# Optimization experiments

Hardware: AMD Instinct MI355X
Metric: run time of the kernel (lower is better)

## Reference

```python
import jax, jax.numpy as jnp
import numpy as np

D_MODEL = 2048
N_HEADS = 16
HEAD_DIM = D_MODEL // N_HEADS
SEQ = 2048
THETA = 10000.0


def rope_tables(head_dim, context_length, theta=THETA):
    inv_freq = 1.0 / theta ** (jnp.arange(0, head_dim, 2, dtype=jnp.float32) / head_dim)
    angles = jnp.arange(context_length, dtype=jnp.float32)[:, None] * inv_freq[None, :]
    angles = jnp.concatenate([angles, angles], axis=1)  # [S, head_dim]
    return jnp.cos(angles), jnp.sin(angles)


def apply_rope(x, cos, sin):
    # x: [B, H, S, Dh]; cos/sin: [S, Dh]
    half = x.shape[-1] // 2
    x1, x2 = x[..., :half], x[..., half:]
    rotated = jnp.concatenate([-x2, x1], axis=-1)
    return x * cos[None, None] + rotated * sin[None, None]


def setup_inputs() -> dict:
    key = jax.random.key(0)
    ks = jax.random.split(key, 5)
    s = 1.0 / np.sqrt(D_MODEL)
    x = jax.random.normal(ks[0], (2, SEQ, D_MODEL), dtype=jnp.float32)
    Wq = jax.random.normal(ks[1], (D_MODEL, D_MODEL), dtype=jnp.float32) * s
    Wk = jax.random.normal(ks[2], (D_MODEL, D_MODEL), dtype=jnp.float32) * s
    Wv = jax.random.normal(ks[3], (D_MODEL, D_MODEL), dtype=jnp.float32) * s
    Wo = jax.random.normal(ks[4], (D_MODEL, D_MODEL), dtype=jnp.float32) * s
    return {"x": x, "Wq": Wq, "Wk": Wk, "Wv": Wv, "Wo": Wo}


def reference(x, Wq, Wk, Wv, Wo):
    B, S, D = x.shape
    cos, sin = rope_tables(HEAD_DIM, SEQ)
    cos, sin = cos[:S], sin[:S]

    def split_heads(t):  # [B,S,D] -> [B,H,S,Dh]
        return t.reshape(B, S, N_HEADS, HEAD_DIM).transpose(0, 2, 1, 3)

    q = apply_rope(split_heads(x @ Wq.T), cos, sin)
    k = apply_rope(split_heads(x @ Wk.T), cos, sin)
    v = split_heads(x @ Wv.T)

    scores = jnp.einsum('bhqd,bhkd->bhqk', q, k) / np.sqrt(HEAD_DIM).astype(np.float32)
    causal = jnp.tril(jnp.ones((S, S), dtype=bool))
    scores = jnp.where(causal[None, None], scores, -jnp.inf)
    weights = jax.nn.softmax(scores, axis=-1)
    ctx = jnp.einsum('bhqk,bhkd->bhqd', weights, v)
    ctx = ctx.transpose(0, 2, 1, 3).reshape(B, S, D)
    return ctx @ Wo.T
```

## Files before the change

kernel.cpp:

```cpp
#include <hip/hip_runtime.h>
#include <hip/hip_bf16.h>
#include <cstdint>
#include <cstddef>

typedef __bf16 bf16;
typedef __bf16 bf16x4 __attribute__((ext_vector_type(4)));
typedef __bf16 bf16x8 __attribute__((ext_vector_type(8)));
typedef float f32x4 __attribute__((ext_vector_type(4)));

#define D_MODEL 2048
#define SEQ     2048
#define NH      16
#define HD      128
#define BATCH   2
#define QKV_LD  6144

#define SBAR()  __builtin_amdgcn_sched_barrier(0)
#define HWBAR() do { SBAR(); __builtin_amdgcn_s_barrier(); SBAR(); } while (0)

__device__ __forceinline__ void gld16(void* lds, const void* g) {
    __builtin_amdgcn_global_load_lds(
        (const __attribute__((address_space(1))) unsigned int*)g,
        (__attribute__((address_space(3))) unsigned int*)lds,
        16, 0, 0);
}

__global__ __launch_bounds__(256) void cvt_f32_bf16(const float* __restrict__ in,
                                                    bf16* __restrict__ out, int n) {
    int i = (blockIdx.x * 256 + threadIdx.x) * 4;
    if (i < n) {
        float4 v = *(const float4*)(in + i);
        out[i + 0] = (bf16)v.x;
        out[i + 1] = (bf16)v.y;
        out[i + 2] = (bf16)v.z;
        out[i + 3] = (bf16)v.w;
    }
}

__global__ __launch_bounds__(256) void rope_tables_k(float* __restrict__ cosd,
                                                     float* __restrict__ sind) {
    int id = blockIdx.x * 256 + threadIdx.x;
    int s = id >> 6, d = id & 63;
    float freq = powf(10000.f, -(float)d * (1.f / 64.f));
    float a = (float)s * freq;
    float sn, c;
    sincosf(a, &sn, &c);
    cosd[id] = c;
    sind[id] = sn;
}

__global__ __launch_bounds__(256) void rope_apply(bf16* __restrict__ T,
                                                  const float* __restrict__ cosd,
                                                  const float* __restrict__ sind,
                                                  float scale, int ld) {
    int id = blockIdx.x * 256 + threadIdx.x;
    int row = id >> 10;
    int p = id & 1023;
    int h = p >> 6, d = p & 63;
    int s = row & (SEQ - 1);
    size_t base = (size_t)row * ld + h * HD + d;
    float x1 = (float)T[base];
    float x2 = (float)T[base + 64];
    float c = cosd[(s << 6) + d];
    float sn = sind[(s << 6) + d];
    T[base]      = (bf16)((x1 * c - x2 * sn) * scale);
    T[base + 64] = (bf16)((x2 * c + x1 * sn) * scale);
}

__global__ __launch_bounds__(256) void transpose_v(const bf16* __restrict__ V,
                                                   bf16* __restrict__ Vt, int ld) {
    __shared__ bf16 t[32][33];
    int s0 = blockIdx.x * 32;
    int d0 = blockIdx.y * 32;
    int bh = blockIdx.z;
    int b = bh >> 4, h = bh & 15;
    int tx = threadIdx.x & 31, ty = threadIdx.x >> 5;
#pragma unroll
    for (int i = 0; i < 32; i += 8)
        t[ty + i][tx] = V[((size_t)(b * SEQ + s0 + ty + i)) * ld + h * HD + d0 + tx];
    __syncthreads();
#pragma unroll
    for (int i = 0; i < 32; i += 8)
        Vt[((size_t)bh * HD + d0 + ty + i) * SEQ + s0 + tx] = t[tx][ty + i];
}

template <int OUTF32>
__global__ __launch_bounds__(512, 2)
void gemm8p(const bf16* __restrict__ A, const bf16* __restrict__ B,
            void* __restrict__ Cout, int M, int N, int K) {
    __shared__ __align__(16) bf16 ldsAB[2][2][2][128 * 64];

    const int nN = N >> 8;
    const int nwg = gridDim.x;
    const int cpx = nwg >> 3;
    const int lin = (blockIdx.x & 7) * cpx + (blockIdx.x >> 3);
    const int m0 = (lin / nN) * 256, n0 = (lin % nN) * 256;

    const int tid = threadIdx.x;
    const int w = tid >> 6, l = tid & 63;
    const int wm = w >> 2, wn = w & 3;
    const int lg = l >> 4, lc = l & 15;
    const int swz = (lc & 7) << 4;
    const int NT = K >> 6;
    const int HMAX = NT * 4;

    f32x4 acc[2][2][4][2] = {};

    auto stage = [&](int H) {
        const int tau = H >> 2, h = H & 3;
        bf16* dst = &ldsAB[tau & 1][h >> 1][h & 1][0];
#pragma unroll
        for (int j = 0; j < 2; ++j) {
            int r = w * 8 + j * 64 + (l >> 3);
            int scb = ((l & 7) * 16) ^ ((r & 7) << 4);
            const bf16* g = (h < 2)
                ? A + (size_t)(m0 + (h & 1) * 128 + r) * K + tau * 64 + (scb >> 1)
                : B + (size_t)(n0 + (h & 1) * 128 + r) * K + tau * 64 + (scb >> 1);
            gld16(dst + (w * 8 + j * 64) * 64, g);
        }
    };

    stage(0); stage(1); stage(2); stage(3); stage(4);
    SBAR();
    asm volatile("s_waitcnt vmcnt(2)" ::: "memory");
    HWBAR();

    for (int t = 0; t < NT; ++t) {
        const int c = t & 1;
        const char* Ab = (const char*)&ldsAB[c][0][wm][0];
        const char* Bb = (const char*)&ldsAB[c][1][wn >> 1][0];
        const int brow0 = (wn & 1) * 64;
        bf16x8 Af[4][2], Bf[2][2][2];

#pragma unroll
        for (int mt = 0; mt < 4; ++mt)
#pragma unroll
            for (int ks = 0; ks < 2; ++ks)
                Af[mt][ks] = *(const bf16x8*)(Ab + (mt * 16 + lc) * 128 + ((ks * 64 + lg * 16) ^ swz));
#pragma unroll
        for (int nt = 0; nt < 2; ++nt)
#pragma unroll
            for (int ks = 0; ks < 2; ++ks)
                Bf[0][nt][ks] = *(const bf16x8*)(Bb + (brow0 + nt * 16 + lc) * 128 + ((ks * 64 + lg * 16) ^ swz));
        { int H = 4 * t + 5; if (H < HMAX) stage(H); }
        HWBAR();
        __builtin_amdgcn_s_setprio(1);
#pragma unroll
        for (int mt = 0; mt < 4; ++mt)
#pragma unroll
            for (int nt = 0; nt < 2; ++nt)
#pragma unroll
                for (int ks = 0; ks < 2; ++ks)
                    acc[0][0][mt][nt] = __builtin_amdgcn_mfma_f32_16x16x32_bf16(Af[mt][ks], Bf[0][nt][ks], acc[0][0][mt][nt], 0, 0, 0);
        __builtin_amdgcn_s_setprio(0);
        HWBAR();

#pragma unroll
        for (int nt = 0; nt < 2; ++nt)
#pragma unroll
            for (int ks = 0; ks < 2; ++ks)
                Bf[1][nt][ks] = *(const bf16x8*)(Bb + (brow0 + 32 + nt * 16 + lc) * 128 + ((ks * 64 + lg * 16) ^ swz));
        { int H = 4 * t + 6; if (H < HMAX) stage(H); }
        HWBAR();
        __builtin_amdgcn_s_setprio(1);
#pragma unroll
        for (int mt = 0; mt < 4; ++mt)
#pragma unroll
            for (int nt = 0; nt < 2; ++nt)
#pragma unroll
                for (int ks = 0; ks < 2; ++ks)
                    acc[0][1][mt][nt] = __builtin_amdgcn_mfma_f32_16x16x32_bf16(Af[mt][ks], Bf[1][nt][ks], acc[0][1][mt][nt], 0, 0, 0);
        __builtin_amdgcn_s_setprio(0);
        HWBAR();

#pragma unroll
        for (int mt = 0; mt < 4; ++mt)
#pragma unroll
            for (int ks = 0; ks < 2; ++ks)
                Af[mt][ks] = *(const bf16x8*)(Ab + (64 + mt * 16 + lc) * 128 + ((ks * 64 + lg * 16) ^ swz));
        { int H = 4 * t + 7; if (H < HMAX) stage(H); }
        HWBAR();
        __builtin_amdgcn_s_setprio(1);
#pragma unroll
        for (int mt = 0; mt < 4; ++mt)
#pragma unroll
            for (int nt = 0; nt < 2; ++nt)
#pragma unroll
                for (int ks = 0; ks < 2; ++ks)
                    acc[1][0][mt][nt] = __builtin_amdgcn_mfma_f32_16x16x32_bf16(Af[mt][ks], Bf[0][nt][ks], acc[1][0][mt][nt], 0, 0, 0);
        __builtin_amdgcn_s_setprio(0);
        HWBAR();

        { int H = 4 * t + 8; if (H < HMAX) stage(H); }
        HWBAR();
        __builtin_amdgcn_s_setprio(1);
#pragma unroll
        for (int mt = 0; mt < 4; ++mt)
#pragma unroll
            for (int nt = 0; nt < 2; ++nt)
#pragma unroll
                for (int ks = 0; ks < 2; ++ks)
                    acc[1][1][mt][nt] = __builtin_amdgcn_mfma_f32_16x16x32_bf16(Af[mt][ks], Bf[1][nt][ks], acc[1][1][mt][nt], 0, 0, 0);
        __builtin_amdgcn_s_setprio(0);
        SBAR();
        asm volatile("s_waitcnt vmcnt(2)" ::: "memory");
        HWBAR();
    }

#pragma unroll
    for (int mq = 0; mq < 2; ++mq)
#pragma unroll
        for (int nq = 0; nq < 2; ++nq)
#pragma unroll
            for (int mt = 0; mt < 4; ++mt)
#pragma unroll
                for (int nt = 0; nt < 2; ++nt)
#pragma unroll
                    for (int rr = 0; rr < 4; ++rr) {
                        size_t row = (size_t)m0 + wm * 128 + mq * 64 + mt * 16 + lg * 4 + rr;
                        size_t col = (size_t)n0 + wn * 64 + nq * 32 + nt * 16 + lc;
                        float v = acc[mq][nq][mt][nt][rr];
                        if (OUTF32) ((float*)Cout)[row * N + col] = v;
                        else        ((bf16*)Cout)[row * N + col] = (bf16)v;
                    }
}

__global__ __launch_bounds__(256)
void flash_attn(const bf16* __restrict__ QKV, const bf16* __restrict__ Vt,
                bf16* __restrict__ O) {
    __shared__ __align__(16) bf16 Ks[2][64 * 128];
    __shared__ __align__(16) bf16 Vs[2][128 * 64];
    __shared__ __align__(16) bf16 p_lds[4][16 * 64];

    const int bid = blockIdx.x;
    const int lin = (bid & 7) * 64 + (bid >> 3);
    const int bh = lin >> 4;
    const int jj = lin & 15;
    const int b = bh >> 4, h = bh & 15;

    const int tid = threadIdx.x;
    const int w = tid >> 6, l = tid & 63;
    const int lg = l >> 4, lc = l & 15;
    const int kswz = (lc & 7) << 4;
    char* pb = (char*)&p_lds[w][0];

    auto stageK = [&](int p, int kb) {
#pragma unroll
        for (int c = 0; c < 4; ++c) {
            int r = c * 16 + w * 4 + (l >> 4);
            int scb = ((l & 15) * 16) ^ ((r & 7) << 4);
            const bf16* g = QKV + ((size_t)(b * SEQ + kb * 64 + r)) * QKV_LD + D_MODEL + h * HD + (scb >> 1);
            gld16(&Ks[p][(c * 16 + w * 4) * 128], g);
        }
    };
    auto stageV = [&](int p, int kb) {
#pragma unroll
        for (int c = 0; c < 4; ++c) {
            int r = c * 32 + w * 8 + (l >> 3);
            int scb = ((l & 7) * 16) ^ ((r & 7) << 4);
            const bf16* g = Vt + ((size_t)bh * HD + r) * SEQ + kb * 64 + (scb >> 1);
            gld16(&Vs[p][(c * 32 + w * 8) * 64], g);
        }
    };

    int cur = 0;
#pragma unroll 1
    for (int ti = 0; ti < 2; ++ti) {
        const int qt = ti ? jj : (31 - jj);
        const int q0 = qt * 64 + w * 16;

        const bf16* qp = QKV + ((size_t)(b * SEQ + q0 + lc)) * QKV_LD + h * HD + lg * 8;
        bf16x8 qf[4];
#pragma unroll
        for (int kc = 0; kc < 4; ++kc) qf[kc] = *(const bf16x8*)(qp + kc * 32);

        f32x4 ctx[8] = {};
        float m_s = -INFINITY, l_s = 0.f;

        stageK(cur, 0);
        stageV(cur, 0);

        for (int kb = 0; kb <= qt; ++kb) {
            __syncthreads();
            if (kb < qt) { stageK(cur ^ 1, kb + 1); stageV(cur ^ 1, kb + 1); }

            const char* kbp = (const char*)&Ks[cur][0];
            f32x4 st[4] = {};
#pragma unroll
            for (int nf = 0; nf < 4; ++nf) {
                int krow = nf * 16 + lc;
#pragma unroll
                for (int kc = 0; kc < 4; ++kc) {
                    bf16x8 kf = *(const bf16x8*)(kbp + krow * 256 + ((kc * 64 + lg * 16) ^ kswz));
                    st[nf] = __builtin_amdgcn_mfma_f32_16x16x32_bf16(kf, qf[kc], st[nf], 0, 0, 0);
                }
            }

            if (kb == qt) {
                int q = q0 + lc;
#pragma unroll
                for (int nf = 0; nf < 4; ++nf) {
                    int key = kb * 64 + nf * 16 + lg * 4;
#pragma unroll
                    for (int r = 0; r < 4; ++r)
                        if (key + r > q) st[nf][r] = -INFINITY;
                }
            }

            float mx = -INFINITY;
#pragma unroll
            for (int nf = 0; nf < 4; ++nf)
#pragma unroll
                for (int r = 0; r < 4; ++r) mx = fmaxf(mx, st[nf][r]);
            mx = fmaxf(mx, __shfl_xor(mx, 16));
            mx = fmaxf(mx, __shfl_xor(mx, 32));
            float mi = fmaxf(m_s, mx);
            float scv = __expf(m_s - mi);
            m_s = mi;

            float rs = 0.f;
#pragma unroll
            for (int nf = 0; nf < 4; ++nf) {
                float p0 = __expf(st[nf][0] - mi);
                float p1 = __expf(st[nf][1] - mi);
                float p2 = __expf(st[nf][2] - mi);
                float p3 = __expf(st[nf][3] - mi);
                rs += (p0 + p1) + (p2 + p3);
                bf16x4 pv = { (bf16)p0, (bf16)p1, (bf16)p2, (bf16)p3 };
                *(bf16x4*)(pb + lc * 128 + ((nf * 32 + lg * 8) ^ kswz)) = pv;
            }
            rs += __shfl_xor(rs, 16);
            rs += __shfl_xor(rs, 32);
            l_s = l_s * scv + rs;

            float scvr[4];
#pragma unroll
            for (int r = 0; r < 4; ++r) scvr[r] = __shfl(scv, lg * 4 + r);
#pragma unroll
            for (int nd = 0; nd < 8; ++nd)
#pragma unroll
                for (int r = 0; r < 4; ++r) ctx[nd][r] *= scvr[r];

            asm volatile("s_waitcnt lgkmcnt(0)" ::: "memory");
            SBAR();
            bf16x8 pa0 = *(const bf16x8*)(pb + lc * 128 + ((lg * 16) ^ kswz));
            bf16x8 pa1 = *(const bf16x8*)(pb + lc * 128 + ((64 + lg * 16) ^ kswz));

            const char* vb = (const char*)&Vs[cur][0];
#pragma unroll
            for (int nd = 0; nd < 8; ++nd) {
                int vrow = nd * 16 + lc;
#pragma unroll
                for (int k2 = 0; k2 < 2; ++k2) {
                    bf16x8 vf = *(const bf16x8*)(vb + vrow * 128 + ((k2 * 64 + lg * 16) ^ kswz));
                    ctx[nd] = __builtin_amdgcn_mfma_f32_16x16x32_bf16(k2 ? pa1 : pa0, vf, ctx[nd], 0, 0, 0);
                }
            }
            cur ^= 1;
        }

        float lr[4];
#pragma unroll
        for (int r = 0; r < 4; ++r) lr[r] = 1.f / __shfl(l_s, lg * 4 + r);
#pragma unroll
        for (int nd = 0; nd < 8; ++nd)
#pragma unroll
            for (int r = 0; r < 4; ++r)
                O[((size_t)(b * SEQ + q0 + lg * 4 + r)) * D_MODEL + h * HD + nd * 16 + lc] =
                    (bf16)(ctx[nd][r] * lr[r]);
    }
}

extern "C" void kernel_launch(void* const* d_in, const int* in_sizes, int n_in,
                              void* d_out, int out_size, void* d_ws, size_t ws_size,
                              hipStream_t stream) {
    const float* x  = (const float*)d_in[0];
    const float* Wq = (const float*)d_in[1];
    const float* Wk = (const float*)d_in[2];
    const float* Wv = (const float*)d_in[3];
    const float* Wo = (const float*)d_in[4];

    char* ws = (char*)d_ws;
    bf16* xb   = (bf16*)(ws + 0);
    bf16* wqkv = (bf16*)(ws + 16777216);
    bf16* wob  = (bf16*)(ws + 41943040);
    bf16* QKV  = (bf16*)(ws + 50331648);
    bf16* Vtb  = (bf16*)(ws + 100663296);
    float* cosd = (float*)(ws + 117440512);
    float* sind = (float*)(ws + 117964800);

    const int NX = BATCH * SEQ * D_MODEL;
    const int NW = D_MODEL * D_MODEL;

    cvt_f32_bf16<<<NX / 1024, 256, 0, stream>>>(x,  xb,  NX);
    cvt_f32_bf16<<<NW / 1024, 256, 0, stream>>>(Wq, wqkv,            NW);
    cvt_f32_bf16<<<NW / 1024, 256, 0, stream>>>(Wk, wqkv + NW,       NW);
    cvt_f32_bf16<<<NW / 1024, 256, 0, stream>>>(Wv, wqkv + 2 * NW,   NW);
    cvt_f32_bf16<<<NW / 1024, 256, 0, stream>>>(Wo, wob,             NW);

    rope_tables_k<<<(SEQ * 64) / 256, 256, 0, stream>>>(cosd, sind);

    gemm8p<0><<<dim3((QKV_LD / 256) * ((BATCH * SEQ) / 256)), 512, 0, stream>>>(
        xb, wqkv, QKV, BATCH * SEQ, QKV_LD, D_MODEL);

    const float qscale = 0.08838834764831845f;
    rope_apply<<<(BATCH * SEQ * 1024) / 256, 256, 0, stream>>>(QKV,           cosd, sind, qscale, QKV_LD);
    rope_apply<<<(BATCH * SEQ * 1024) / 256, 256, 0, stream>>>(QKV + D_MODEL, cosd, sind, 1.0f,   QKV_LD);

    transpose_v<<<dim3(SEQ / 32, HD / 32, BATCH * NH), 256, 0, stream>>>(QKV + 2 * D_MODEL, Vtb, QKV_LD);

    flash_attn<<<dim3(512), 256, 0, stream>>>(QKV, Vtb, xb );

    gemm8p<1><<<dim3((D_MODEL / 256) * ((BATCH * SEQ) / 256)), 512, 0, stream>>>(
        xb, wob, d_out, BATCH * SEQ, D_MODEL, D_MODEL);
}
```

Baseline: 296.0 us.

## Merge conversion kernels, remap GEMM tiles per XCD, restructure GEMM prefetch

Five f32-to-bf16 conversion launches become one kernel that indexes x and the four weight matrices from a single flat range; the workspace layout is contiguous, so the outputs land in the same places. The GEMM now assigns each XCD a compact rectangular block of output tiles, chosen to minimise rows plus columns, to improve L2 reuse of A and B. The staging schedule changes from one quarter-tile per phase to staging the B halves of the next k-step and the A halves two k-steps ahead. This removes a barrier and uses different vmcnt waits, which deepens the prefetch but adds pipeline-depth and synchronisation risk.

```diff
diff --git a/kernel.cpp b/kernel.cpp
--- a/kernel.cpp
+++ b/kernel.cpp
@@ -25,16 +25,25 @@
         16, 0, 0);
 }
 
-__global__ __launch_bounds__(256) void cvt_f32_bf16(const float* __restrict__ in,
-                                                    bf16* __restrict__ out, int n) {
+__global__ __launch_bounds__(256) void cvt_all(const float* __restrict__ x,
+                                               const float* __restrict__ Wq,
+                                               const float* __restrict__ Wk,
+                                               const float* __restrict__ Wv,
+                                               const float* __restrict__ Wo,
+                                               bf16* __restrict__ out) {
     int i = (blockIdx.x * 256 + threadIdx.x) * 4;
-    if (i < n) {
-        float4 v = *(const float4*)(in + i);
-        out[i + 0] = (bf16)v.x;
-        out[i + 1] = (bf16)v.y;
-        out[i + 2] = (bf16)v.z;
-        out[i + 3] = (bf16)v.w;
+    const float* src;
+    int off;
+    if (i < 8388608) { src = x; off = i; }
+    else {
+        int j = i - 8388608;
+        int seg = j >> 22;
+        src = (seg == 0) ? Wq : (seg == 1) ? Wk : (seg == 2) ? Wv : Wo;
+        off = j & 4194303;
     }
+    float4 v = *(const float4*)(src + off);
+    bf16* o = out + i;
+    o[0] = (bf16)v.x; o[1] = (bf16)v.y; o[2] = (bf16)v.z; o[3] = (bf16)v.w;
 }
 
 __global__ __launch_bounds__(256) void rope_tables_k(float* __restrict__ cosd,
@@ -90,11 +99,27 @@
             void* __restrict__ Cout, int M, int N, int K) {
     __shared__ __align__(16) bf16 ldsAB[2][2][2][128 * 64];
 
-    const int nN = N >> 8;
-    const int nwg = gridDim.x;
-    const int cpx = nwg >> 3;
-    const int lin = (blockIdx.x & 7) * cpx + (blockIdx.x >> 3);
-    const int m0 = (lin / nN) * 256, n0 = (lin % nN) * 256;
+    const int nM = M >> 8, nN = N >> 8;
+    const int cpx = (nM * nN) >> 3;
+
+    int bchm = 0, bchn = 0, best = 0x7fffffff;
+    for (int d = 1; d <= cpx; ++d) {
+        if (cpx % d) continue;
+        int cm = cpx / d;
+        if (nM % cm || nN % d) continue;
+        if (cm + d < best) { best = cm + d; bchm = cm; bchn = d; }
+    }
+    int mt0, nt0;
+    if (bchm) {
+        const int ncn = nN / bchn;
+        const int xcd = blockIdx.x & 7, loc = blockIdx.x >> 3;
+        mt0 = (xcd / ncn) * bchm + loc / bchn;
+        nt0 = (xcd % ncn) * bchn + loc % bchn;
+    } else {
+        const int lin = (blockIdx.x & 7) * cpx + (blockIdx.x >> 3);
+        mt0 = lin / nN; nt0 = lin % nN;
+    }
+    const int m0 = mt0 * 256, n0 = nt0 * 256;
 
     const int tid = threadIdx.x;
     const int w = tid >> 6, l = tid & 63;
@@ -102,27 +127,25 @@
     const int lg = l >> 4, lc = l & 15;
     const int swz = (lc & 7) << 4;
     const int NT = K >> 6;
-    const int HMAX = NT * 4;
 
     f32x4 acc[2][2][4][2] = {};
 
-    auto stage = [&](int H) {
-        const int tau = H >> 2, h = H & 3;
-        bf16* dst = &ldsAB[tau & 1][h >> 1][h & 1][0];
+    auto stageU = [&](int tau, int u) {
+        bf16* dst = &ldsAB[tau & 1][u >> 1][u & 1][0];
+        const bf16* src = (u < 2) ? A + (size_t)(m0 + (u & 1) * 128) * K
+                                  : B + (size_t)(n0 + (u & 1) * 128) * K;
 #pragma unroll
         for (int j = 0; j < 2; ++j) {
             int r = w * 8 + j * 64 + (l >> 3);
             int scb = ((l & 7) * 16) ^ ((r & 7) << 4);
-            const bf16* g = (h < 2)
-                ? A + (size_t)(m0 + (h & 1) * 128 + r) * K + tau * 64 + (scb >> 1)
-                : B + (size_t)(n0 + (h & 1) * 128 + r) * K + tau * 64 + (scb >> 1);
-            gld16(dst + (w * 8 + j * 64) * 64, g);
+            gld16(dst + (w * 8 + j * 64) * 64, src + (size_t)r * K + tau * 64 + (scb >> 1));
         }
     };
 
-    stage(0); stage(1); stage(2); stage(3); stage(4);
+    stageU(0, 0); stageU(0, 1); stageU(0, 2); stageU(0, 3);
+    stageU(1, 0); stageU(1, 1);
     SBAR();
-    asm volatile("s_waitcnt vmcnt(2)" ::: "memory");
+    asm volatile("s_waitcnt vmcnt(4)" ::: "memory");
     HWBAR();
 
     for (int t = 0; t < NT; ++t) {
@@ -142,7 +165,7 @@
 #pragma unroll
             for (int ks = 0; ks < 2; ++ks)
                 Bf[0][nt][ks] = *(const bf16x8*)(Bb + (brow0 + nt * 16 + lc) * 128 + ((ks * 64 + lg * 16) ^ swz));
-        { int H = 4 * t + 5; if (H < HMAX) stage(H); }
+        if (t + 1 < NT) stageU(t + 1, 2);
         HWBAR();
         __builtin_amdgcn_s_setprio(1);
 #pragma unroll
@@ -160,7 +183,7 @@
 #pragma unroll
             for (int ks = 0; ks < 2; ++ks)
                 Bf[1][nt][ks] = *(const bf16x8*)(Bb + (brow0 + 32 + nt * 16 + lc) * 128 + ((ks * 64 + lg * 16) ^ swz));
-        { int H = 4 * t + 6; if (H < HMAX) stage(H); }
+        if (t + 1 < NT) stageU(t + 1, 3);
         HWBAR();
         __builtin_amdgcn_s_setprio(1);
 #pragma unroll
@@ -178,7 +201,6 @@
 #pragma unroll
             for (int ks = 0; ks < 2; ++ks)
                 Af[mt][ks] = *(const bf16x8*)(Ab + (64 + mt * 16 + lc) * 128 + ((ks * 64 + lg * 16) ^ swz));
-        { int H = 4 * t + 7; if (H < HMAX) stage(H); }
         HWBAR();
         __builtin_amdgcn_s_setprio(1);
 #pragma unroll
@@ -191,8 +213,7 @@
         __builtin_amdgcn_s_setprio(0);
         HWBAR();
 
-        { int H = 4 * t + 8; if (H < HMAX) stage(H); }
-        HWBAR();
+        if (t + 2 < NT) { stageU(t + 2, 0); stageU(t + 2, 1); }
         __builtin_amdgcn_s_setprio(1);
 #pragma unroll
         for (int mt = 0; mt < 4; ++mt)
@@ -203,7 +224,8 @@
                     acc[1][1][mt][nt] = __builtin_amdgcn_mfma_f32_16x16x32_bf16(Af[mt][ks], Bf[1][nt][ks], acc[1][1][mt][nt], 0, 0, 0);
         __builtin_amdgcn_s_setprio(0);
         SBAR();
-        asm volatile("s_waitcnt vmcnt(2)" ::: "memory");
+        if (t + 2 < NT) asm volatile("s_waitcnt vmcnt(4)" ::: "memory");
+        else            asm volatile("s_waitcnt vmcnt(0)" ::: "memory");
         HWBAR();
     }
 
@@ -389,14 +411,7 @@
     float* cosd = (float*)(ws + 117440512);
     float* sind = (float*)(ws + 117964800);
 
-    const int NX = BATCH * SEQ * D_MODEL;
-    const int NW = D_MODEL * D_MODEL;
-
-    cvt_f32_bf16<<<NX / 1024, 256, 0, stream>>>(x,  xb,  NX);
-    cvt_f32_bf16<<<NW / 1024, 256, 0, stream>>>(Wq, wqkv,            NW);
-    cvt_f32_bf16<<<NW / 1024, 256, 0, stream>>>(Wk, wqkv + NW,       NW);
-    cvt_f32_bf16<<<NW / 1024, 256, 0, stream>>>(Wv, wqkv + 2 * NW,   NW);
-    cvt_f32_bf16<<<NW / 1024, 256, 0, stream>>>(Wo, wob,             NW);
+    cvt_all<<<25165824 / 1024, 256, 0, stream>>>(x, Wq, Wk, Wv, Wo, xb);
 
     rope_tables_k<<<(SEQ * 64) / 256, 256, 0, stream>>>(cosd, sind);
 
```

Result: slower. 311.0 us (+5.1%).

## Merge conversion launches, fix GEMM tail wait, use 128-tile GEMM for output projection

Applied to the files above, without the earlier changes.

Replaces the five f32-to-bf16 conversion launches with one kernel that picks the source tensor by index, relying on the workspace buffers being contiguous. Changes the final loop iteration of the pipelined GEMM to wait for all outstanding loads. Adds a simpler double-buffered 128x128 GEMM and uses it for the output projection, so that smaller GEMM gets more blocks to fill the GPU. The new GEMM has a shallower pipeline and more uncoalesced output stores, which may offset the occupancy gain.

```diff
diff --git a/kernel.cpp b/kernel.cpp
--- a/kernel.cpp
+++ b/kernel.cpp
@@ -25,16 +25,25 @@
         16, 0, 0);
 }
 
-__global__ __launch_bounds__(256) void cvt_f32_bf16(const float* __restrict__ in,
-                                                    bf16* __restrict__ out, int n) {
+__global__ __launch_bounds__(256) void cvt_all(const float* __restrict__ x,
+                                               const float* __restrict__ Wq,
+                                               const float* __restrict__ Wk,
+                                               const float* __restrict__ Wv,
+                                               const float* __restrict__ Wo,
+                                               bf16* __restrict__ out) {
     int i = (blockIdx.x * 256 + threadIdx.x) * 4;
-    if (i < n) {
-        float4 v = *(const float4*)(in + i);
-        out[i + 0] = (bf16)v.x;
-        out[i + 1] = (bf16)v.y;
-        out[i + 2] = (bf16)v.z;
-        out[i + 3] = (bf16)v.w;
+    const float* src;
+    int off;
+    if (i < 8388608) { src = x; off = i; }
+    else {
+        int j = i - 8388608;
+        int seg = j >> 22;
+        src = (seg == 0) ? Wq : (seg == 1) ? Wk : (seg == 2) ? Wv : Wo;
+        off = j & 4194303;
     }
+    float4 v = *(const float4*)(src + off);
+    bf16* o = out + i;
+    o[0] = (bf16)v.x; o[1] = (bf16)v.y; o[2] = (bf16)v.z; o[3] = (bf16)v.w;
 }
 
 __global__ __launch_bounds__(256) void rope_tables_k(float* __restrict__ cosd,
@@ -203,7 +212,8 @@
                     acc[1][1][mt][nt] = __builtin_amdgcn_mfma_f32_16x16x32_bf16(Af[mt][ks], Bf[1][nt][ks], acc[1][1][mt][nt], 0, 0, 0);
         __builtin_amdgcn_s_setprio(0);
         SBAR();
-        asm volatile("s_waitcnt vmcnt(2)" ::: "memory");
+        if (t + 2 < NT) asm volatile("s_waitcnt vmcnt(2)" ::: "memory");
+        else            asm volatile("s_waitcnt vmcnt(0)" ::: "memory");
         HWBAR();
     }
 
@@ -223,6 +233,68 @@
                         if (OUTF32) ((float*)Cout)[row * N + col] = v;
                         else        ((bf16*)Cout)[row * N + col] = (bf16)v;
                     }
+}
+
+template <int OUTF32>
+__global__ __launch_bounds__(256)
+void gemm_nt(const bf16* __restrict__ A, const bf16* __restrict__ B,
+             void* __restrict__ Cout, int M, int N, int K) {
+    __shared__ bf16 As[2][128 * 32];
+    __shared__ bf16 Bs[2][128 * 32];
+    const int m0 = blockIdx.y * 128, n0 = blockIdx.x * 128;
+    const int tid = threadIdx.x;
+    const int w = tid >> 6, l = tid & 63;
+    const int wr = w >> 1, wc = w & 1;
+    const int lg = l >> 4, lc = l & 15;
+
+    f32x4 acc[4][4] = {};
+    const int NT = K >> 5;
+
+    auto stage = [&](int p, int t) {
+#pragma unroll
+        for (int c = 0; c < 2; ++c) {
+            int reg = w * 2 + c;
+            const bf16* ga = A + (size_t)(m0 + reg * 16 + (l >> 2)) * K + t * 32 + (l & 3) * 8;
+            const bf16* gb = B + (size_t)(n0 + reg * 16 + (l >> 2)) * K + t * 32 + (l & 3) * 8;
+            gld16(&As[p][reg * 512], ga);
+            gld16(&Bs[p][reg * 512], gb);
+        }
+    };
+
+    stage(0, 0);
+    int cur = 0;
+    for (int t = 0; t < NT; ++t) {
+        __syncthreads();
+        if (t + 1 < NT) stage(cur ^ 1, t + 1);
+        bf16x8 af[4], bfr[4];
+#pragma unroll
+        for (int m = 0; m < 4; ++m)
+            af[m] = *(const bf16x8*)&As[cur][(wr * 64 + m * 16 + lc) * 32 + lg * 8];
+#pragma unroll
+        for (int n = 0; n < 4; ++n)
+            bfr[n] = *(const bf16x8*)&Bs[cur][(wc * 64 + n * 16 + lc) * 32 + lg * 8];
+#pragma unroll
+        for (int m = 0; m < 4; ++m)
+#pragma unroll
+            for (int n = 0; n < 4; ++n)
+                acc[m][n] = __builtin_amdgcn_mfma_f32_16x16x32_bf16(af[m], bfr[n], acc[m][n], 0, 0, 0);
+        cur ^= 1;
+    }
+
+#pragma unroll
+    for (int m = 0; m < 4; ++m)
+#pragma unroll
+        for (int n = 0; n < 4; ++n)
+#pragma unroll
+            for (int r = 0; r < 4; ++r) {
+                size_t row = (size_t)m0 + wr * 64 + m * 16 + lg * 4 + r;
+                size_t col = (size_t)n0 + wc * 64 + n * 16 + lc;
+                float v = acc[m][n][r];
+                if (OUTF32)
+                    ((float*)Cout)[row * N + col] = v;
+                else
+                    ((bf16*)Cout)[row * N + col] = (bf16)v;
+            }
 }
 
 __global__ __launch_bounds__(256)
@@ -389,18 +461,11 @@
     float* cosd = (float*)(ws + 117440512);
     float* sind = (float*)(ws + 117964800);
 
-    const int NX = BATCH * SEQ * D_MODEL;
-    const int NW = D_MODEL * D_MODEL;
-
-    cvt_f32_bf16<<<NX / 1024, 256, 0, stream>>>(x,  xb,  NX);
-    cvt_f32_bf16<<<NW / 1024, 256, 0, stream>>>(Wq, wqkv,            NW);
-    cvt_f32_bf16<<<NW / 1024, 256, 0, stream>>>(Wk, wqkv + NW,       NW);
-    cvt_f32_bf16<<<NW / 1024, 256, 0, stream>>>(Wv, wqkv + 2 * NW,   NW);
-    cvt_f32_bf16<<<NW / 1024, 256, 0, stream>>>(Wo, wob,             NW);
+    cvt_all<<<25165824 / 1024, 256, 0, stream>>>(x, Wq, Wk, Wv, Wo, xb);
 
     rope_tables_k<<<(SEQ * 64) / 256, 256, 0, stream>>>(cosd, sind);
 
-    gemm8p<0><<<dim3((QKV_LD / 256) * ((BATCH * SEQ) / 256)), 512, 0, stream>>>(
+    gemm8p<0><<<dim3(384), 512, 0, stream>>>(
         xb, wqkv, QKV, BATCH * SEQ, QKV_LD, D_MODEL);
 
     const float qscale = 0.08838834764831845f;
@@ -411,6 +476,6 @@
 
     flash_attn<<<dim3(512), 256, 0, stream>>>(QKV, Vtb, xb );
 
-    gemm8p<1><<<dim3((D_MODEL / 256) * ((BATCH * SEQ) / 256)), 512, 0, stream>>>(
+    gemm_nt<1><<<dim3(D_MODEL / 128, (BATCH * SEQ) / 128), 256, 0, stream>>>(
         xb, wob, d_out, BATCH * SEQ, D_MODEL, D_MODEL);
 }
```

After: 284.2 us. -4.0%, faster.
